# Optimization experiments

Measured on AMD Instinct MI355X. Metric: run time of the kernel, lower is better.

Reference implementation:

```python
import jax, jax.numpy as jnp
import numpy as np

B, T, HID = 2, 2048, 3840
H, KV, D = 16, 8, 256
EPS = 1e-6
WINDOW = 1024
THETA_LOCAL = 10000.0
THETA_GLOBAL = 1000000.0


def _rope_tables(theta, t, d):
    inv_freq = 1.0 / (theta ** (jnp.arange(0, d, 2, dtype=jnp.float32) / d))  # (d/2,)
    ang = jnp.arange(t, dtype=jnp.float32)[:, None] * inv_freq[None, :]        # (T, d/2)
    return jnp.cos(ang), jnp.sin(ang)


def setup_inputs() -> dict:
    key = jax.random.key(0)
    ks = jax.random.split(key, 8)
    x = jax.random.normal(ks[0], (B, T, HID), dtype=jnp.float32)
    wq = jax.random.normal(ks[1], (H * D, HID), dtype=jnp.float32) * 0.02
    wk = jax.random.normal(ks[2], (KV * D, HID), dtype=jnp.float32) * 0.02
    wv = jax.random.normal(ks[3], (KV * D, HID), dtype=jnp.float32) * 0.02
    wo = jax.random.normal(ks[4], (HID, H * D), dtype=jnp.float32) * 0.02
    q_norm_w = 1.0 + jax.random.normal(ks[5], (D,), dtype=jnp.float32) * 0.02
    k_norm_w = 1.0 + jax.random.normal(ks[6], (D,), dtype=jnp.float32) * 0.02
    cos_g, sin_g = _rope_tables(THETA_GLOBAL, T, D)
    cos_l, sin_l = _rope_tables(THETA_LOCAL, T, D)
    # causal + sliding-window(1024) additive float mask, shape (1,1,T,T)
    i = jnp.arange(T)[:, None]
    j = jnp.arange(T)[None, :]
    allowed = (j <= i) & (i - j < WINDOW)
    attention_mask = jnp.where(allowed, 0.0, -1e9).astype(jnp.float32)[None, None]
    return {"x": x, "cos_global": cos_g, "sin_global": sin_g, "cos_local": cos_l,
            "sin_local": sin_l, "attention_mask": attention_mask,
            "wq": wq, "wk": wk, "wv": wv, "wo": wo,
            "q_norm_w": q_norm_w, "k_norm_w": k_norm_w}


def _rms_norm(x, w):
    # add=False variant: x * rsqrt(mean(x^2)+eps) * w, computed in fp32
    norm = jax.lax.rsqrt(jnp.mean(jnp.square(x), axis=-1, keepdims=True) + EPS)
    return x * norm * w


def _apply_rope(x, cos, sin):
    # x: (B, H, T, D); cos/sin: (T, D/2)
    t = x.shape[2]
    c = cos[:t][None, None]
    s = sin[:t][None, None]
    x1, x2 = x[..., : x.shape[-1] // 2], x[..., x.shape[-1] // 2 :]
    return jnp.concatenate([x1 * c - x2 * s, x2 * c + x1 * s], axis=-1)


def reference(x, cos_global, sin_global, cos_local, sin_local, attention_mask,
              wq, wk, wv, wo, q_norm_w, k_norm_w):
    b, t, _ = x.shape
    q = (x @ wq.T).reshape(b, t, H, D).transpose(0, 2, 1, 3)   # (B,H,T,D)
    k = (x @ wk.T).reshape(b, t, KV, D).transpose(0, 2, 1, 3)  # (B,KV,T,D)
    v = (x @ wv.T).reshape(b, t, KV, D).transpose(0, 2, 1, 3)
    q = _rms_norm(q, q_norm_w)
    k = _rms_norm(k, k_norm_w)
    # layer_idx=0 -> sliding-window layer -> local rope
    q = _apply_rope(q, cos_local, sin_local)
    k = _apply_rope(k, cos_local, sin_local)
    rep = H // KV
    k = jnp.repeat(k, rep, axis=1)  # repeat_interleave over head dim
    v = jnp.repeat(v, rep, axis=1)
    scale = 1.0 / jnp.sqrt(jnp.float32(D))
    scores = jnp.einsum("bhqd,bhkd->bhqk", q, k) * scale + attention_mask
    attn = jax.nn.softmax(scores, axis=-1)
    out = jnp.einsum("bhqk,bhkd->bhqd", attn, v)
    out = out.transpose(0, 2, 1, 3).reshape(b, t, H * D)
    return out @ wo.T
```

## Files before the change

### kernel.cpp

```cpp
#include <hip/hip_runtime.h>
#include <hip/hip_bf16.h>

typedef __hip_bfloat16 BF;
typedef __attribute__((ext_vector_type(8))) short short8;
typedef __attribute__((ext_vector_type(4))) float f32x4;

#define DEV __device__ __forceinline__

DEV void gll16(const BF* g, BF* l) {
  __builtin_amdgcn_global_load_lds(
      (const __attribute__((address_space(1))) void*)g,
      (__attribute__((address_space(3))) void*)l, 16, 0, 0);
}

DEV unsigned short bfbits(float f) {
  BF b = __float2bfloat16(f);
  return *reinterpret_cast<unsigned short*>(&b);
}

DEV ushort4 cvt4(const float4 v) {
  return make_ushort4(bfbits(v.x), bfbits(v.y), bfbits(v.z), bfbits(v.w));
}

__global__ void cvt_fused(const float* __restrict__ x, const float* __restrict__ wq,
                          const float* __restrict__ wk, const float* __restrict__ wv,
                          const float* __restrict__ wo,
                          BF* __restrict__ Xbf, BF* __restrict__ Wqkv, BF* __restrict__ Wo) {
  const int stride = gridDim.x * blockDim.x;
  for (int i = blockIdx.x * blockDim.x + threadIdx.x; i < 15728640; i += stride) {
    if (i < 11796480) {
      const float* src;
      ushort4* dst;
      int off;
      if (i < 3932160)      { src = x;  off = i;           dst = (ushort4*)Xbf; }
      else if (i < 7864320) { src = wq; off = i - 3932160; dst = (ushort4*)Wqkv; }
      else if (i < 9830400) { src = wk; off = i - 7864320; dst = (ushort4*)(Wqkv + 4096 * 3840); }
      else                  { src = wv; off = i - 9830400; dst = (ushort4*)(Wqkv + 6144 * 3840); }
      dst[off] = cvt4(((const float4*)src)[off]);
    } else {
      const int off = i - 11796480;
      const int r = off >> 10, c = off & 1023;
      ((ushort4*)Wo)[r * 1040 + c] = cvt4(((const float4*)wo)[off]);
    }
  }
}

#define PHASE(MH, KK, READB, STAGE, TAIL)                                            \
  {                                                                                  \
    short8 af[4];                                                                    \
    const BF* Ap = Ax + (KK)*8192;                                                   \
    _Pragma("unroll") for (int m = 0; m < 4; ++m)                                    \
        af[m] = *(const short8*)&Ap[(wm*128 + (MH)*64 + m*16 + l15) * 32 + rd8];     \
    if (READB) {                                                                     \
      const BF* Bp = Bx + (KK)*8192;                                                 \
      _Pragma("unroll") for (int n = 0; n < 4; ++n)                                  \
          breg[n] = *(const short8*)&Bp[(wn*64 + n*16 + l15) * 32 + rd8];            \
    }                                                                                \
    STAGE                                                                            \
    __builtin_amdgcn_s_barrier();                                                    \
    asm volatile("s_waitcnt lgkmcnt(0)" ::: "memory");                               \
    __builtin_amdgcn_sched_barrier(0);                                               \
    __builtin_amdgcn_s_setprio(1);                                                   \
    _Pragma("unroll") for (int m = 0; m < 4; ++m)                                    \
      _Pragma("unroll") for (int n = 0; n < 4; ++n)                                  \
        acc[(MH)*4 + m][n] =                                                         \
            __builtin_amdgcn_mfma_f32_16x16x32_bf16(af[m], breg[n], acc[(MH)*4+m][n], 0, 0, 0); \
    __builtin_amdgcn_s_setprio(0);                                                   \
    TAIL                                                                             \
    __builtin_amdgcn_s_barrier();                                                    \
  }

#define STG2(SRC, RST, DST) { gll16((SRC), (DST)); gll16((SRC) + (RST), (DST) + 4096); }

template <typename CT>
DEV void gemm256_body(const BF* __restrict__ A, const BF* __restrict__ Bm,
                      CT* __restrict__ C, const int M, const int N, const int K,
                      const int lda, const int ldb) {
  extern __shared__ __align__(16) BF lds[];
  BF* ldsA = lds;
  BF* ldsB = lds + 32768;
  const int ntl = N >> 8;
  const int mtl = M >> 8;
  int mt, nt;
  if (mtl == 16 && ntl == 32) {
    const int x = blockIdx.x & 7;
    const int c = blockIdx.x >> 3;
    mt = ((x >> 2) << 3) + (c >> 3);
    nt = ((x & 3) << 3) + (c & 7);
  } else {
    const int cpx = gridDim.x >> 3;
    const int swzb = (blockIdx.x & 7) * cpx + (blockIdx.x >> 3);
    mt = swzb / ntl;
    nt = swzb % ntl;
  }
  const int m0 = mt << 8, n0 = nt << 8;
  const int tid = threadIdx.x, lane = tid & 63, w = tid >> 6;
  const int l15 = lane & 15, g = lane >> 4;
  const int wm = w >> 2, wn = w & 3;
  const int rd8 = (g ^ ((l15 >> 1) & 3)) << 3;
  const int trow = tid >> 2;
  const int scol = ((lane & 3) ^ ((lane >> 3) & 3)) << 3;
  const BF* aS = A + (size_t)(m0 + trow) * lda + scol;
  const BF* bS = Bm + (size_t)(n0 + trow) * ldb + scol;
  const size_t rstpA = (size_t)128 * lda;
  const size_t rstpB = (size_t)128 * ldb;
  BF* dA = ldsA + w * 512;
  BF* dB = ldsB + w * 512;
  const int NT = K >> 6;

  f32x4 acc[8][4];
#pragma unroll
  for (int m = 0; m < 8; ++m)
#pragma unroll
    for (int n = 0; n < 4; ++n) acc[m][n] = (f32x4){0.f, 0.f, 0.f, 0.f};
  short8 breg[4];

  STG2(aS, rstpA, dA);
  STG2(bS, rstpB, dB);
  STG2(aS + 32, rstpA, dA + 8192);
  STG2(bS + 32, rstpB, dB + 8192);
  STG2(aS + 64, rstpA, dA + 16384);
  STG2(bS + 64, rstpB, dB + 16384);
  asm volatile("s_waitcnt vmcnt(8)" ::: "memory");
  __builtin_amdgcn_sched_barrier(0);
  __builtin_amdgcn_s_barrier();

  for (int t = 0; t < NT; ++t) {
    const int bX = (t & 1) << 14;
    const int bY = bX ^ 16384;
    const BF* Ax = ldsA + bX;
    const BF* Bx = ldsB + bX;
    const int kc1 = (t + 1) << 6, kc2 = (t + 2) << 6;
    const bool s1 = (t + 1 < NT), s2 = (t + 2 < NT);
    PHASE(0, 0, 1, if (s1) STG2(aS + kc1 + 32, rstpA, dA + bY + 8192);, )
    PHASE(1, 0, 0, if (s1) STG2(bS + kc1 + 32, rstpB, dB + bY + 8192);,
          { asm volatile("s_waitcnt vmcnt(8)" ::: "memory");
            __builtin_amdgcn_sched_barrier(0); } )
    PHASE(0, 1, 1, if (s2) STG2(aS + kc2, rstpA, dA + bX);, )
    PHASE(1, 1, 0, if (s2) STG2(bS + kc2, rstpB, dB + bX);,
          if (s2) { asm volatile("s_waitcnt vmcnt(8)" ::: "memory");
                    __builtin_amdgcn_sched_barrier(0); }
          else    { asm volatile("s_waitcnt vmcnt(0)" ::: "memory");
                    __builtin_amdgcn_sched_barrier(0); } )
  }

#pragma unroll
  for (int mi = 0; mi < 8; ++mi) {
    const int gr = m0 + wm * 128 + mi * 16 + g * 4;
#pragma unroll
    for (int n = 0; n < 4; ++n) {
      const int gc = n0 + wn * 64 + n * 16 + l15;
#pragma unroll
      for (int r = 0; r < 4; ++r) {
        const float v = acc[mi][n][r];
        if constexpr (sizeof(CT) == 2)
          C[(size_t)(gr + r) * N + gc] = __float2bfloat16(v);
        else
          C[(size_t)(gr + r) * N + gc] = v;
      }
    }
  }
}

__global__ __launch_bounds__(512, 2) void gemm_qkv(const BF* __restrict__ A,
                                                   const BF* __restrict__ Bm,
                                                   BF* __restrict__ C,
                                                   int M, int N, int K, int lda, int ldb) {
  gemm256_body<BF>(A, Bm, C, M, N, K, lda, ldb);
}
__global__ __launch_bounds__(512, 2) void gemm_out(const BF* __restrict__ A,
                                                   const BF* __restrict__ Bm,
                                                   float* __restrict__ C,
                                                   int M, int N, int K, int lda, int ldb) {
  gemm256_body<float>(A, Bm, C, M, N, K, lda, ldb);
}

__global__ __launch_bounds__(256) void rmsrope(const BF* __restrict__ C1,
                                               BF* __restrict__ Qo, BF* __restrict__ Ko,
                                               const float* __restrict__ cosl,
                                               const float* __restrict__ sinl,
                                               const float* __restrict__ qw,
                                               const float* __restrict__ kw) {
  const int gwid = (blockIdx.x * 256 + threadIdx.x) >> 6;
  const int lane = threadIdx.x & 63;
  const int slot = gwid % 24;
  const int bt = gwid / 24;
  const int b = bt >> 11, t = bt & 2047;
  const BF* src;
  BF* dst;
  const float* wgt;
  if (slot < 16) {
    src = C1 + (size_t)bt * 8192 + slot * 256;
    dst = Qo + ((size_t)(b * 16 + slot) * 2048 + t) * 256;
    wgt = qw;
  } else {
    const int kv = slot - 16;
    src = C1 + (size_t)bt * 8192 + 4096 + kv * 256;
    dst = Ko + ((size_t)(b * 8 + kv) * 2048 + t) * 256;
    wgt = kw;
  }
  const int d2 = lane * 2;
  const ushort2 lo = *(const ushort2*)((const unsigned short*)src + d2);
  const ushort2 hi = *(const ushort2*)((const unsigned short*)src + 128 + d2);
  float x0 = __bfloat162float(*(const BF*)&lo.x);
  float x1 = __bfloat162float(*(const BF*)&lo.y);
  float x2 = __bfloat162float(*(const BF*)&hi.x);
  float x3 = __bfloat162float(*(const BF*)&hi.y);
  float ss = x0 * x0 + x1 * x1 + x2 * x2 + x3 * x3;
#pragma unroll
  for (int mm = 32; mm >= 1; mm >>= 1) ss += __shfl_xor(ss, mm);
  const float nrm = rsqrtf(ss * (1.f / 256.f) + 1e-6f);
  const float2 wlo = *(const float2*)(wgt + d2);
  const float2 whi = *(const float2*)(wgt + 128 + d2);
  x0 *= nrm * wlo.x;
  x1 *= nrm * wlo.y;
  x2 *= nrm * whi.x;
  x3 *= nrm * whi.y;
  const float2 c = *(const float2*)(cosl + t * 128 + d2);
  const float2 s = *(const float2*)(sinl + t * 128 + d2);
  ushort2 olo, ohi;
  olo.x = bfbits(x0 * c.x - x2 * s.x);
  olo.y = bfbits(x1 * c.y - x3 * s.y);
  ohi.x = bfbits(x2 * c.x + x0 * s.x);
  ohi.y = bfbits(x3 * c.y + x1 * s.y);
  *(ushort2*)((unsigned short*)dst + d2) = olo;
  *(ushort2*)((unsigned short*)dst + 128 + d2) = ohi;
}

__global__ __launch_bounds__(256) void vtrans(const BF* __restrict__ C1, BF* __restrict__ Vt) {
  __shared__ BF tile[64][68];
  const int bz = blockIdx.z;
  const int tt = blockIdx.x;
  const int dt = blockIdx.y;
  const int tid = threadIdx.x;
  const int r16 = tid >> 4;
  const int c16 = tid & 15;
  const int b = bz >> 3, kv = bz & 7;
#pragma unroll
  for (int p = 0; p < 4; ++p) {
    const int tr = p * 16 + r16;
    const int t = tt * 64 + tr;
    const int d = dt * 64 + c16 * 4;
    *(ushort4*)&tile[tr][c16 * 4] =
        *(const ushort4*)&C1[((size_t)(b * 2048 + t)) * 8192 + 6144 + kv * 256 + d];
  }
  __syncthreads();
#pragma unroll
  for (int p = 0; p < 4; ++p) {
    const int dr = p * 16 + r16;
    const int d = dt * 64 + dr;
    const int t4 = c16 * 4;
    ushort4 o;
    o.x = *(const unsigned short*)&tile[t4 + 0][dr];
    o.y = *(const unsigned short*)&tile[t4 + 1][dr];
    o.z = *(const unsigned short*)&tile[t4 + 2][dr];
    o.w = *(const unsigned short*)&tile[t4 + 3][dr];
    *(ushort4*)&Vt[((size_t)bz * 256 + d) * 2048 + tt * 64 + t4] = o;
  }
}

__global__ __launch_bounds__(512, 1) void attn_fwd(const BF* __restrict__ Q,
                                                   const BF* __restrict__ K,
                                                   const BF* __restrict__ Vt,
                                                   BF* __restrict__ O) {
  __shared__ __align__(16) BF Ks[64 * 256];
  __shared__ __align__(16) BF Vs[256 * 64];
  __shared__ __align__(16) BF Ps[8][1024];
  const int tid = threadIdx.x;
  const int lane = tid & 63;
  const int w = tid >> 6;
  const int wh = w >> 2;
  const int wq = w & 3;
  const int l15 = lane & 15;
  const int g = lane >> 4;
  const int qt = blockIdx.x;
  const int bp = blockIdx.y;
  const int b = bp >> 3, kvh = bp & 7;
  const int h = kvh * 2 + wh;
  const int q0 = qt << 6;
  const BF* Qb = Q + ((size_t)(b * 16 + h) * 2048 + q0) * 256;
  const BF* Kb = K + (size_t)(b * 8 + kvh) * 2048 * 256;
  const BF* Vb = Vt + (size_t)(b * 8 + kvh) * 256 * 2048;

  short8 qf[8];
  {
    const BF* qr = Qb + (wq * 16 + l15) * 256 + g * 8;
#pragma unroll
    for (int kk = 0; kk < 8; ++kk) qf[kk] = *(const short8*)(qr + kk * 32);
  }
  f32x4 oacc[16];
#pragma unroll
  for (int i = 0; i < 16; ++i) oacc[i] = (f32x4){0.f, 0.f, 0.f, 0.f};
  float m_r[4] = {-1e30f, -1e30f, -1e30f, -1e30f};
  float l_r[4] = {0.f, 0.f, 0.f, 0.f};

  const int kt_lo = (q0 > 1023) ? ((q0 - 1023) >> 6) : 0;
  for (int kt = kt_lo; kt <= qt; ++kt) {
    const int tk = kt << 6;
#pragma unroll
    for (int i = 0; i < 4; ++i) {
      const int li = w * 4 + i;
      {
        const int row = li * 2 + (lane >> 5);
        const int ch = lane & 31;
        gll16(Kb + (size_t)(tk + row) * 256 + ((ch ^ (row & 7)) << 3), Ks + li * 512);
      }
      {
        const int row = li * 8 + (lane >> 3);
        const int ch = lane & 7;
        gll16(Vb + (size_t)row * 2048 + tk + ((ch ^ (row & 7)) << 3), Vs + li * 512);
      }
    }
    __syncthreads();

    f32x4 sa[4];
#pragma unroll
    for (int i2 = 0; i2 < 4; ++i2) sa[i2] = (f32x4){0.f, 0.f, 0.f, 0.f};
#pragma unroll
    for (int kk = 0; kk < 8; ++kk) {
      const int d = kk * 32 + g * 8;
#pragma unroll
      for (int blk = 0; blk < 4; ++blk) {
        const int row = blk * 16 + l15;
        const short8 kf = *(const short8*)&Ks[row * 256 + (d ^ ((row & 7) << 3))];
        sa[blk] = __builtin_amdgcn_mfma_f32_16x16x32_bf16(qf[kk], kf, sa[blk], 0, 0, 0);
      }
    }

    float al4[4];
#pragma unroll
    for (int r = 0; r < 4; ++r) {
      const int qi = q0 + wq * 16 + g * 4 + r;
      float pv[4];
      float tmax = -1e30f;
#pragma unroll
      for (int blk = 0; blk < 4; ++blk) {
        const int ki = tk + blk * 16 + l15;
        float sv = sa[blk][r] * 0.0625f;
        const bool ok = (ki <= qi) && (qi - ki < 1024);
        sv = ok ? sv : -1e30f;
        pv[blk] = sv;
        tmax = fmaxf(tmax, sv);
      }
#pragma unroll
      for (int mm = 1; mm < 16; mm <<= 1) tmax = fmaxf(tmax, __shfl_xor(tmax, mm));
      const float mn = fmaxf(m_r[r], tmax);
      const float alpha = __expf(m_r[r] - mn);
      float tsum = 0.f;
#pragma unroll
      for (int blk = 0; blk < 4; ++blk) {
        const float p = __expf(pv[blk] - mn);
        pv[blk] = p;
        tsum += p;
      }
#pragma unroll
      for (int mm = 1; mm < 16; mm <<= 1) tsum += __shfl_xor(tsum, mm);
      l_r[r] = l_r[r] * alpha + tsum;
      m_r[r] = mn;
      al4[r] = alpha;
      const int prow = g * 4 + r;
#pragma unroll
      for (int blk = 0; blk < 4; ++blk) {
        const int col = blk * 16 + l15;
        Ps[w][prow * 64 + (col ^ ((prow & 7) << 3))] = __float2bfloat16(pv[blk]);
      }
    }
#pragma unroll
    for (int db = 0; db < 16; ++db)
#pragma unroll
      for (int r = 0; r < 4; ++r) oacc[db][r] *= al4[r];

#pragma unroll
    for (int kk2 = 0; kk2 < 2; ++kk2) {
      const int k8 = kk2 * 32 + g * 8;
      const short8 pf = *(const short8*)&Ps[w][l15 * 64 + (k8 ^ ((l15 & 7) << 3))];
#pragma unroll
      for (int db = 0; db < 16; ++db) {
        const int vrow = db * 16 + l15;
        const short8 vf = *(const short8*)&Vs[vrow * 64 + (k8 ^ ((vrow & 7) << 3))];
        oacc[db] = __builtin_amdgcn_mfma_f32_16x16x32_bf16(pf, vf, oacc[db], 0, 0, 0);
      }
    }
    __syncthreads();
  }

#pragma unroll
  for (int r = 0; r < 4; ++r) l_r[r] = 1.f / l_r[r];
  const size_t orow0 = (size_t)(b * 2048 + q0 + wq * 16 + g * 4);
#pragma unroll
  for (int r = 0; r < 4; ++r) {
    BF* op = O + (orow0 + r) * 4160 + h * 256 + l15;
#pragma unroll
    for (int db = 0; db < 16; ++db) op[db * 16] = __float2bfloat16(oacc[db][r] * l_r[r]);
  }
}

extern "C" void kernel_launch(void* const* d_in, const int* in_sizes, int n_in,
                              void* d_out, int out_size, void* d_ws, size_t ws_size,
                              hipStream_t stream) {
  (void)in_sizes; (void)n_in; (void)out_size;
  const float* x    = (const float*)d_in[0];
  const float* cosl = (const float*)d_in[3];
  const float* sinl = (const float*)d_in[4];
  const float* wq   = (const float*)d_in[6];
  const float* wk   = (const float*)d_in[7];
  const float* wv   = (const float*)d_in[8];
  const float* wo   = (const float*)d_in[9];
  const float* qw   = (const float*)d_in[10];
  const float* kw   = (const float*)d_in[11];
  float* out = (float*)d_out;
  char* ws = (char*)d_ws;
  if (ws_size < 193429504ull) return;

  BF* Wqkv = (BF*)(ws + 0);
  BF* Xbf  = (BF*)(ws + 62914560);
  BF* C1   = (BF*)(ws + 94371840);
  BF* Qb   = (BF*)(ws + 0);
  BF* Kb   = (BF*)(ws + 33554432);
  BF* Vt   = (BF*)(ws + 62914560);
  BF* AO   = (BF*)(ws + 94371840);
  BF* Wo   = (BF*)(ws + 161480704);

  hipFuncSetAttribute(reinterpret_cast<const void*>(gemm_qkv),
                      hipFuncAttributeMaxDynamicSharedMemorySize, 131072);
  hipFuncSetAttribute(reinterpret_cast<const void*>(gemm_out),
                      hipFuncAttributeMaxDynamicSharedMemorySize, 131072);

  cvt_fused<<<2048, 256, 0, stream>>>(x, wq, wk, wv, wo, Xbf, Wqkv, Wo);

  gemm_qkv<<<512, 512, 131072, stream>>>(Xbf, Wqkv, C1, 4096, 8192, 3840, 3840, 3840);
  rmsrope<<<24576, 256, 0, stream>>>(C1, Qb, Kb, cosl, sinl, qw, kw);
  vtrans<<<dim3(32, 4, 16), 256, 0, stream>>>(C1, Vt);
  attn_fwd<<<dim3(32, 16), 512, 0, stream>>>(Qb, Kb, Vt, AO);
  gemm_out<<<240, 512, 131072, stream>>>(AO, Wo, out, 4096, 3840, 4096, 4160, 4160);
}
```

Before: 570.8 us.

## Use 16-wave 1024-thread GEMM blocks with smaller per-wave accumulator tiles

Both GEMM kernels keep the 256x256 block tile but now launch 1024 threads (16 waves) instead of 512. Each wave computes a 64x64 subtile with a 4x4 accumulator array instead of 128x64 with 8x4. Each thread issues one global-to-LDS load per operand per stage instead of two, and the phase schedule and vmcnt waits are rewritten to match. The aim is more waves to hide LDS and memory latency and lower register pressure per wave. The cost is more LDS fragment reads per MFMA, since each wave now reloads B for half the M work, and heavier barrier synchronisation across 16 waves.

```diff
diff --git a/kernel.cpp b/kernel.cpp
--- a/kernel.cpp
+++ b/kernel.cpp
@@ -45,32 +45,33 @@
   }
 }
 
-#define PHASE(MH, KK, READB, STAGE, TAIL)                                            \
-  {                                                                                  \
-    short8 af[4];                                                                    \
-    const BF* Ap = Ax + (KK)*8192;                                                   \
-    _Pragma("unroll") for (int m = 0; m < 4; ++m)                                    \
-        af[m] = *(const short8*)&Ap[(wm*128 + (MH)*64 + m*16 + l15) * 32 + rd8];     \
-    if (READB) {                                                                     \
-      const BF* Bp = Bx + (KK)*8192;                                                 \
-      _Pragma("unroll") for (int n = 0; n < 4; ++n)                                  \
-          breg[n] = *(const short8*)&Bp[(wn*64 + n*16 + l15) * 32 + rd8];            \
-    }                                                                                \
-    STAGE                                                                            \
-    __builtin_amdgcn_s_barrier();                                                    \
-    asm volatile("s_waitcnt lgkmcnt(0)" ::: "memory");                               \
-    __builtin_amdgcn_sched_barrier(0);                                               \
-    __builtin_amdgcn_s_setprio(1);                                                   \
-    _Pragma("unroll") for (int m = 0; m < 4; ++m)                                    \
-      _Pragma("unroll") for (int n = 0; n < 4; ++n)                                  \
-        acc[(MH)*4 + m][n] =                                                         \
-            __builtin_amdgcn_mfma_f32_16x16x32_bf16(af[m], breg[n], acc[(MH)*4+m][n], 0, 0, 0); \
-    __builtin_amdgcn_s_setprio(0);                                                   \
-    TAIL                                                                             \
-    __builtin_amdgcn_s_barrier();                                                    \
-  }
-
-#define STG2(SRC, RST, DST) { gll16((SRC), (DST)); gll16((SRC) + (RST), (DST) + 4096); }
+#define WAITV(N)                                                                      \
+  asm volatile("s_waitcnt vmcnt(" #N ")" ::: "memory");                               \
+  __builtin_amdgcn_sched_barrier(0);
+#define BAR() __builtin_amdgcn_s_barrier();
+#define STGU(KC, BOFF)                                                                \
+  { gll16(aS + (KC), ldsA + (BOFF) + w * 512);                                        \
+    gll16(bS + (KC), ldsB + (BOFF) + w * 512); }
+#define GPHASE(KK, STAGE, TAIL)                                                       \
+  {                                                                                   \
+    short8 af[4], bf[4];                                                              \
+    _Pragma("unroll") for (int m_ = 0; m_ < 4; ++m_)                                  \
+        af[m_] = *(const short8*)&ldsA[bX + (KK)*8192 + (wm*64 + m_*16 + l15)*32 + rd8]; \
+    _Pragma("unroll") for (int n_ = 0; n_ < 4; ++n_)                                  \
+        bf[n_] = *(const short8*)&ldsB[bX + (KK)*8192 + (wn*64 + n_*16 + l15)*32 + rd8]; \
+    STAGE                                                                             \
+    __builtin_amdgcn_s_barrier();                                                     \
+    asm volatile("s_waitcnt lgkmcnt(0)" ::: "memory");                                \
+    __builtin_amdgcn_sched_barrier(0);                                                \
+    __builtin_amdgcn_s_setprio(1);                                                    \
+    _Pragma("unroll") for (int m_ = 0; m_ < 4; ++m_)                                  \
+      _Pragma("unroll") for (int n_ = 0; n_ < 4; ++n_)                                 \
+        acc[m_][n_] =                                                                 \
+            __builtin_amdgcn_mfma_f32_16x16x32_bf16(af[m_], bf[n_], acc[m_][n_], 0, 0, 0); \
+    __builtin_amdgcn_s_setprio(0);                                                    \
+    TAIL                                                                              \
+    __builtin_amdgcn_s_barrier();                                                     \
+  }
 
 template <typename CT>
 DEV void gemm256_body(const BF* __restrict__ A, const BF* __restrict__ Bm,
@@ -102,51 +103,34 @@
   const int scol = ((lane & 3) ^ ((lane >> 3) & 3)) << 3;
   const BF* aS = A + (size_t)(m0 + trow) * lda + scol;
   const BF* bS = Bm + (size_t)(n0 + trow) * ldb + scol;
-  const size_t rstpA = (size_t)128 * lda;
-  const size_t rstpB = (size_t)128 * ldb;
-  BF* dA = ldsA + w * 512;
-  BF* dB = ldsB + w * 512;
   const int NT = K >> 6;
 
-  f32x4 acc[8][4];
-#pragma unroll
-  for (int m = 0; m < 8; ++m)
+  f32x4 acc[4][4];
+#pragma unroll
+  for (int m = 0; m < 4; ++m)
 #pragma unroll
     for (int n = 0; n < 4; ++n) acc[m][n] = (f32x4){0.f, 0.f, 0.f, 0.f};
-  short8 breg[4];
-
-  STG2(aS, rstpA, dA);
-  STG2(bS, rstpB, dB);
-  STG2(aS + 32, rstpA, dA + 8192);
-  STG2(bS + 32, rstpB, dB + 8192);
-  STG2(aS + 64, rstpA, dA + 16384);
-  STG2(bS + 64, rstpB, dB + 16384);
-  asm volatile("s_waitcnt vmcnt(8)" ::: "memory");
-  __builtin_amdgcn_sched_barrier(0);
-  __builtin_amdgcn_s_barrier();
+
+  STGU(0, 0);
+  STGU(32, 8192);
+  STGU(64, 16384);
+  WAITV(4)
+  BAR()
 
   for (int t = 0; t < NT; ++t) {
     const int bX = (t & 1) << 14;
     const int bY = bX ^ 16384;
-    const BF* Ax = ldsA + bX;
-    const BF* Bx = ldsB + bX;
     const int kc1 = (t + 1) << 6, kc2 = (t + 2) << 6;
     const bool s1 = (t + 1 < NT), s2 = (t + 2 < NT);
-    PHASE(0, 0, 1, if (s1) STG2(aS + kc1 + 32, rstpA, dA + bY + 8192);, )
-    PHASE(1, 0, 0, if (s1) STG2(bS + kc1 + 32, rstpB, dB + bY + 8192);,
-          { asm volatile("s_waitcnt vmcnt(8)" ::: "memory");
-            __builtin_amdgcn_sched_barrier(0); } )
-    PHASE(0, 1, 1, if (s2) STG2(aS + kc2, rstpA, dA + bX);, )
-    PHASE(1, 1, 0, if (s2) STG2(bS + kc2, rstpB, dB + bX);,
-          if (s2) { asm volatile("s_waitcnt vmcnt(8)" ::: "memory");
-                    __builtin_amdgcn_sched_barrier(0); }
-          else    { asm volatile("s_waitcnt vmcnt(0)" ::: "memory");
-                    __builtin_amdgcn_sched_barrier(0); } )
-  }
-
-#pragma unroll
-  for (int mi = 0; mi < 8; ++mi) {
-    const int gr = m0 + wm * 128 + mi * 16 + g * 4;
+    GPHASE(0, if (s1) STGU(kc1 + 32, bY + 8192);,
+           if (s1) { WAITV(4) } else { WAITV(0) })
+    GPHASE(1, if (s2) STGU(kc2, bX);,
+           if (s2) { WAITV(4) } else if (s1) { WAITV(2) })
+  }
+
+#pragma unroll
+  for (int mi = 0; mi < 4; ++mi) {
+    const int gr = m0 + wm * 64 + mi * 16 + g * 4;
 #pragma unroll
     for (int n = 0; n < 4; ++n) {
       const int gc = n0 + wn * 64 + n * 16 + l15;
@@ -162,16 +146,16 @@
   }
 }
 
-__global__ __launch_bounds__(512, 2) void gemm_qkv(const BF* __restrict__ A,
-                                                   const BF* __restrict__ Bm,
-                                                   BF* __restrict__ C,
-                                                   int M, int N, int K, int lda, int ldb) {
+__global__ __launch_bounds__(1024, 4) void gemm_qkv(const BF* __restrict__ A,
+                                                    const BF* __restrict__ Bm,
+                                                    BF* __restrict__ C,
+                                                    int M, int N, int K, int lda, int ldb) {
   gemm256_body<BF>(A, Bm, C, M, N, K, lda, ldb);
 }
-__global__ __launch_bounds__(512, 2) void gemm_out(const BF* __restrict__ A,
-                                                   const BF* __restrict__ Bm,
-                                                   float* __restrict__ C,
-                                                   int M, int N, int K, int lda, int ldb) {
+__global__ __launch_bounds__(1024, 4) void gemm_out(const BF* __restrict__ A,
+                                                    const BF* __restrict__ Bm,
+                                                    float* __restrict__ C,
+                                                    int M, int N, int K, int lda, int ldb) {
   gemm256_body<float>(A, Bm, C, M, N, K, lda, ldb);
 }
 
@@ -428,9 +412,9 @@
 
   cvt_fused<<<2048, 256, 0, stream>>>(x, wq, wk, wv, wo, Xbf, Wqkv, Wo);
 
-  gemm_qkv<<<512, 512, 131072, stream>>>(Xbf, Wqkv, C1, 4096, 8192, 3840, 3840, 3840);
+  gemm_qkv<<<512, 1024, 131072, stream>>>(Xbf, Wqkv, C1, 4096, 8192, 3840, 3840, 3840);
   rmsrope<<<24576, 256, 0, stream>>>(C1, Qb, Kb, cosl, sinl, qw, kw);
   vtrans<<<dim3(32, 4, 16), 256, 0, stream>>>(C1, Vt);
   attn_fwd<<<dim3(32, 16), 512, 0, stream>>>(Qb, Kb, Vt, AO);
-  gemm_out<<<240, 512, 131072, stream>>>(AO, Wo, out, 4096, 3840, 4096, 4160, 4160);
-}
+  gemm_out<<<240, 1024, 131072, stream>>>(AO, Wo, out, 4096, 3840, 4096, 4160, 4160);
+}
```

New measurement: 598.5 us. 1.05x slower.

## Fuse RMSNorm and RoPE into QKV GEMM epilogue via permuted weight rows

Applied to the files above, without the earlier changes.

Removes the separate rmsrope kernel by computing the per-head RMS norm and rotary embedding directly in the QKV GEMM epilogue. Q and K weight rows are permuted during conversion so that each wave holds matching rotate-half pairs, with the row sum of squares reduced across waves in LDS. Only V is written to an intermediate buffer, which cuts the round trip of the full QKV output through global memory. The cost is a heavier epilogue with an extra barrier and scattered 2-byte stores, plus index arithmetic in the conversion kernel.

```diff
diff --git a/kernel.cpp b/kernel.cpp
--- a/kernel.cpp
+++ b/kernel.cpp
@@ -20,6 +20,11 @@
 
 DEV ushort4 cvt4(const float4 v) {
   return make_ushort4(bfbits(v.x), bfbits(v.y), bfbits(v.z), bfbits(v.w));
+}
+
+DEV int rope_perm(int d) {
+  return (d < 128) ? ((d >> 5) * 64 + (d & 31))
+                   : (((d - 128) >> 5) * 64 + 32 + ((d - 128) & 31));
 }
 
 __global__ void cvt_fused(const float* __restrict__ x, const float* __restrict__ wq,
@@ -28,15 +33,21 @@
                           BF* __restrict__ Xbf, BF* __restrict__ Wqkv, BF* __restrict__ Wo) {
   const int stride = gridDim.x * blockDim.x;
   for (int i = blockIdx.x * blockDim.x + threadIdx.x; i < 15728640; i += stride) {
-    if (i < 11796480) {
-      const float* src;
-      ushort4* dst;
-      int off;
-      if (i < 3932160)      { src = x;  off = i;           dst = (ushort4*)Xbf; }
-      else if (i < 7864320) { src = wq; off = i - 3932160; dst = (ushort4*)Wqkv; }
-      else if (i < 9830400) { src = wk; off = i - 7864320; dst = (ushort4*)(Wqkv + 4096 * 3840); }
-      else                  { src = wv; off = i - 9830400; dst = (ushort4*)(Wqkv + 6144 * 3840); }
-      dst[off] = cvt4(((const float4*)src)[off]);
+    if (i < 3932160) {
+      ((ushort4*)Xbf)[i] = cvt4(((const float4*)x)[i]);
+    } else if (i < 7864320) {
+      const int off = i - 3932160;
+      const int row = off / 960, col = off - row * 960;
+      const int nrow = (row & ~255) | rope_perm(row & 255);
+      ((ushort4*)Wqkv)[nrow * 960 + col] = cvt4(((const float4*)wq)[off]);
+    } else if (i < 9830400) {
+      const int off = i - 7864320;
+      const int row = off / 960, col = off - row * 960;
+      const int nrow = (row & ~255) | rope_perm(row & 255);
+      ((ushort4*)(Wqkv + 4096 * 3840))[nrow * 960 + col] = cvt4(((const float4*)wk)[off]);
+    } else if (i < 11796480) {
+      const int off = i - 9830400;
+      ((ushort4*)(Wqkv + 6144 * 3840))[off] = cvt4(((const float4*)wv)[off]);
     } else {
       const int off = i - 11796480;
       const int r = off >> 10, c = off & 1023;
@@ -72,10 +83,13 @@
 
 #define STG2(SRC, RST, DST) { gll16((SRC), (DST)); gll16((SRC) + (RST), (DST) + 4096); }
 
-template <typename CT>
+template <typename CT, int MODE>
 DEV void gemm256_body(const BF* __restrict__ A, const BF* __restrict__ Bm,
                       CT* __restrict__ C, const int M, const int N, const int K,
-                      const int lda, const int ldb) {
+                      const int lda, const int ldb,
+                      BF* __restrict__ Qb, BF* __restrict__ Kb,
+                      const float* __restrict__ cosl, const float* __restrict__ sinl,
+                      const float* __restrict__ qw, const float* __restrict__ kw) {
   extern __shared__ __align__(16) BF lds[];
   BF* ldsA = lds;
   BF* ldsB = lds + 32768;
@@ -144,19 +158,86 @@
                     __builtin_amdgcn_sched_barrier(0); } )
   }
 
-#pragma unroll
-  for (int mi = 0; mi < 8; ++mi) {
-    const int gr = m0 + wm * 128 + mi * 16 + g * 4;
-#pragma unroll
-    for (int n = 0; n < 4; ++n) {
-      const int gc = n0 + wn * 64 + n * 16 + l15;
-#pragma unroll
-      for (int r = 0; r < 4; ++r) {
-        const float v = acc[mi][n][r];
-        if constexpr (sizeof(CT) == 2)
-          C[(size_t)(gr + r) * N + gc] = __float2bfloat16(v);
-        else
-          C[(size_t)(gr + r) * N + gc] = v;
+  if constexpr (MODE == 0) {
+#pragma unroll
+    for (int mi = 0; mi < 8; ++mi) {
+      const int gr = m0 + wm * 128 + mi * 16 + g * 4;
+#pragma unroll
+      for (int n = 0; n < 4; ++n) {
+        const int gc = n0 + wn * 64 + n * 16 + l15;
+#pragma unroll
+        for (int r = 0; r < 4; ++r)
+          C[(size_t)(gr + r) * N + gc] = acc[mi][n][r];
+      }
+    }
+  } else {
+    if (nt >= 24) {
+#pragma unroll
+      for (int mi = 0; mi < 8; ++mi) {
+        const int gr = m0 + wm * 128 + mi * 16 + g * 4;
+#pragma unroll
+        for (int n = 0; n < 4; ++n) {
+          const int gc = n0 - 6144 + wn * 64 + n * 16 + l15;
+#pragma unroll
+          for (int r = 0; r < 4; ++r)
+            C[(size_t)(gr + r) * 2048 + gc] = __float2bfloat16(acc[mi][n][r]);
+        }
+      }
+    } else {
+      const bool isq = (nt < 16);
+      const int head = isq ? nt : (nt - 16);
+      const float* wgt = isq ? qw : kw;
+      float* red = (float*)lds;
+      __builtin_amdgcn_s_barrier();
+#pragma unroll
+      for (int mi = 0; mi < 8; ++mi) {
+        float ps[4];
+#pragma unroll
+        for (int r = 0; r < 4; ++r) {
+          float s = 0.f;
+#pragma unroll
+          for (int n = 0; n < 4; ++n) s += acc[mi][n][r] * acc[mi][n][r];
+#pragma unroll
+          for (int mm = 1; mm < 16; mm <<= 1) s += __shfl_xor(s, mm);
+          ps[r] = s;
+        }
+        if (l15 == 0) {
+          const int rb = wm * 128 + mi * 16 + g * 4;
+#pragma unroll
+          for (int r = 0; r < 4; ++r) red[(rb + r) * 4 + wn] = ps[r];
+        }
+      }
+      __syncthreads();
+      float rms[8][4];
+#pragma unroll
+      for (int mi = 0; mi < 8; ++mi)
+#pragma unroll
+        for (int r = 0; r < 4; ++r) {
+          const int row = wm * 128 + mi * 16 + g * 4 + r;
+          const float4 p = *(const float4*)&red[row * 4];
+          rms[mi][r] = rsqrtf((p.x + p.y + p.z + p.w) * (1.f / 256.f) + 1e-6f);
+        }
+#pragma unroll
+      for (int mi = 0; mi < 8; ++mi) {
+#pragma unroll
+        for (int r = 0; r < 4; ++r) {
+          const int grow = m0 + wm * 128 + mi * 16 + g * 4 + r;
+          const int tt = grow & 2047, bb = grow >> 11;
+          const float rm = rms[mi][r];
+          BF* orow = (isq ? Qb + ((size_t)(bb * 16 + head) * 2048 + tt) * 256
+                          : Kb + ((size_t)(bb * 8 + head) * 2048 + tt) * 256);
+#pragma unroll
+          for (int n = 0; n < 2; ++n) {
+            const int dlo = wn * 32 + n * 16 + l15;
+            const float cc = cosl[tt * 128 + dlo];
+            const float ss = sinl[tt * 128 + dlo];
+            const float xl = acc[mi][n][r] * rm * wgt[dlo];
+            const float xh = acc[mi][n + 2][r] * rm * wgt[dlo + 128];
+            const int cbase = wn * 64 + n * 16 + l15;
+            orow[cbase]      = __float2bfloat16(xl * cc - xh * ss);
+            orow[cbase + 32] = __float2bfloat16(xh * cc + xl * ss);
+          }
+        }
       }
     }
   }
@@ -164,70 +245,24 @@
 
 __global__ __launch_bounds__(512, 2) void gemm_qkv(const BF* __restrict__ A,
                                                    const BF* __restrict__ Bm,
-                                                   BF* __restrict__ C,
+                                                   BF* __restrict__ C1v,
+                                                   BF* __restrict__ Qb, BF* __restrict__ Kb,
+                                                   const float* __restrict__ cosl,
+                                                   const float* __restrict__ sinl,
+                                                   const float* __restrict__ qw,
+                                                   const float* __restrict__ kw,
                                                    int M, int N, int K, int lda, int ldb) {
-  gemm256_body<BF>(A, Bm, C, M, N, K, lda, ldb);
+  gemm256_body<BF, 1>(A, Bm, C1v, M, N, K, lda, ldb, Qb, Kb, cosl, sinl, qw, kw);
 }
 __global__ __launch_bounds__(512, 2) void gemm_out(const BF* __restrict__ A,
                                                    const BF* __restrict__ Bm,
                                                    float* __restrict__ C,
                                                    int M, int N, int K, int lda, int ldb) {
-  gemm256_body<float>(A, Bm, C, M, N, K, lda, ldb);
-}
-
-__global__ __launch_bounds__(256) void rmsrope(const BF* __restrict__ C1,
-                                               BF* __restrict__ Qo, BF* __restrict__ Ko,
-                                               const float* __restrict__ cosl,
-                                               const float* __restrict__ sinl,
-                                               const float* __restrict__ qw,
-                                               const float* __restrict__ kw) {
-  const int gwid = (blockIdx.x * 256 + threadIdx.x) >> 6;
-  const int lane = threadIdx.x & 63;
-  const int slot = gwid % 24;
-  const int bt = gwid / 24;
-  const int b = bt >> 11, t = bt & 2047;
-  const BF* src;
-  BF* dst;
-  const float* wgt;
-  if (slot < 16) {
-    src = C1 + (size_t)bt * 8192 + slot * 256;
-    dst = Qo + ((size_t)(b * 16 + slot) * 2048 + t) * 256;
-    wgt = qw;
-  } else {
-    const int kv = slot - 16;
-    src = C1 + (size_t)bt * 8192 + 4096 + kv * 256;
-    dst = Ko + ((size_t)(b * 8 + kv) * 2048 + t) * 256;
-    wgt = kw;
-  }
-  const int d2 = lane * 2;
-  const ushort2 lo = *(const ushort2*)((const unsigned short*)src + d2);
-  const ushort2 hi = *(const ushort2*)((const unsigned short*)src + 128 + d2);
-  float x0 = __bfloat162float(*(const BF*)&lo.x);
-  float x1 = __bfloat162float(*(const BF*)&lo.y);
-  float x2 = __bfloat162float(*(const BF*)&hi.x);
-  float x3 = __bfloat162float(*(const BF*)&hi.y);
-  float ss = x0 * x0 + x1 * x1 + x2 * x2 + x3 * x3;
-#pragma unroll
-  for (int mm = 32; mm >= 1; mm >>= 1) ss += __shfl_xor(ss, mm);
-  const float nrm = rsqrtf(ss * (1.f / 256.f) + 1e-6f);
-  const float2 wlo = *(const float2*)(wgt + d2);
-  const float2 whi = *(const float2*)(wgt + 128 + d2);
-  x0 *= nrm * wlo.x;
-  x1 *= nrm * wlo.y;
-  x2 *= nrm * whi.x;
-  x3 *= nrm * whi.y;
-  const float2 c = *(const float2*)(cosl + t * 128 + d2);
-  const float2 s = *(const float2*)(sinl + t * 128 + d2);
-  ushort2 olo, ohi;
-  olo.x = bfbits(x0 * c.x - x2 * s.x);
-  olo.y = bfbits(x1 * c.y - x3 * s.y);
-  ohi.x = bfbits(x2 * c.x + x0 * s.x);
-  ohi.y = bfbits(x3 * c.y + x1 * s.y);
-  *(ushort2*)((unsigned short*)dst + d2) = olo;
-  *(ushort2*)((unsigned short*)dst + 128 + d2) = ohi;
-}
-
-__global__ __launch_bounds__(256) void vtrans(const BF* __restrict__ C1, BF* __restrict__ Vt) {
+  gemm256_body<float, 0>(A, Bm, C, M, N, K, lda, ldb,
+                         nullptr, nullptr, nullptr, nullptr, nullptr, nullptr);
+}
+
+__global__ __launch_bounds__(256) void vtrans(const BF* __restrict__ C1v, BF* __restrict__ Vt) {
   __shared__ BF tile[64][68];
   const int bz = blockIdx.z;
   const int tt = blockIdx.x;
@@ -242,7 +277,7 @@
     const int t = tt * 64 + tr;
     const int d = dt * 64 + c16 * 4;
     *(ushort4*)&tile[tr][c16 * 4] =
-        *(const ushort4*)&C1[((size_t)(b * 2048 + t)) * 8192 + 6144 + kv * 256 + d];
+        *(const ushort4*)&C1v[((size_t)(b * 2048 + t)) * 2048 + kv * 256 + d];
   }
   __syncthreads();
 #pragma unroll
@@ -414,12 +449,12 @@
 
   BF* Wqkv = (BF*)(ws + 0);
   BF* Xbf  = (BF*)(ws + 62914560);
-  BF* C1   = (BF*)(ws + 94371840);
-  BF* Qb   = (BF*)(ws + 0);
-  BF* Kb   = (BF*)(ws + 33554432);
-  BF* Vt   = (BF*)(ws + 62914560);
-  BF* AO   = (BF*)(ws + 94371840);
+  BF* Qb   = (BF*)(ws + 94371840);
+  BF* Kb   = (BF*)(ws + 127926272);
+  BF* C1v  = (BF*)(ws + 144703488);
   BF* Wo   = (BF*)(ws + 161480704);
+  BF* Vt   = (BF*)(ws + 0);
+  BF* AO   = (BF*)(ws + 16777216);
 
   hipFuncSetAttribute(reinterpret_cast<const void*>(gemm_qkv),
                       hipFuncAttributeMaxDynamicSharedMemorySize, 131072);
@@ -428,9 +463,9 @@
 
   cvt_fused<<<2048, 256, 0, stream>>>(x, wq, wk, wv, wo, Xbf, Wqkv, Wo);
 
-  gemm_qkv<<<512, 512, 131072, stream>>>(Xbf, Wqkv, C1, 4096, 8192, 3840, 3840, 3840);
-  rmsrope<<<24576, 256, 0, stream>>>(C1, Qb, Kb, cosl, sinl, qw, kw);
-  vtrans<<<dim3(32, 4, 16), 256, 0, stream>>>(C1, Vt);
+  gemm_qkv<<<512, 512, 131072, stream>>>(Xbf, Wqkv, C1v, Qb, Kb, cosl, sinl, qw, kw,
+                                         4096, 8192, 3840, 3840, 3840);
+  vtrans<<<dim3(32, 4, 16), 256, 0, stream>>>(C1v, Vt);
   attn_fwd<<<dim3(32, 16), 512, 0, stream>>>(Qb, Kb, Vt, AO);
   gemm_out<<<240, 512, 131072, stream>>>(AO, Wo, out, 4096, 3840, 4096, 4160, 4160);
 }
```

After: 568.0 us. No clear change (-0.5%).
